# Performance work log

Measured on AMD Instinct MI355X. Metric: run time of the kernel, lower is better.

## Reference

```python
import jax, jax.numpy as jnp
import numpy as np

D = 1024
HEADS = 16
HEAD_DIM = D // HEADS
B = 4
L = 1024


def setup_inputs() -> dict:
    key = jax.random.key(0)
    kq, kk, kv, kw, kb = jax.random.split(key, 5)
    Q = jax.random.normal(kq, (B, L, D), dtype=jnp.float32)
    K = jax.random.normal(kk, (B, L, D), dtype=jnp.float32)
    V = jax.random.normal(kv, (B, L, D), dtype=jnp.float32)
    # Output projection H: torch nn.Linear(D, D) -> weight (D, D), bias (D,)
    lim = 1.0 / np.sqrt(D)
    W_H = jax.random.uniform(kw, (D, D), minval=-lim, maxval=lim, dtype=jnp.float32)
    b_H = jax.random.uniform(kb, (D,), minval=-lim, maxval=lim, dtype=jnp.float32)
    mask = 0  # falsy -> no masking branch, matching `if mask` in the source
    return {"Q": Q, "K": K, "V": V, "W_H": W_H, "b_H": b_H, "mask": mask}


def reference(Q, K, V, W_H, b_H, mask):
    batch, q_len, _ = Q.shape
    k_len = K.shape[1]
    Qh = Q.reshape(batch, q_len, HEADS, HEAD_DIM)
    Kh = K.reshape(batch, k_len, HEADS, HEAD_DIM)
    Vh = V.reshape(batch, k_len, HEADS, HEAD_DIM)
    scores = jnp.einsum('bqhd,bkhd->bhqk', Qh, Kh)  # [B,H,Lq,Lk]
    if mask:  # mask is a Python scalar (0 -> skip), as in source
        scores = jnp.where(mask == 0, -jnp.inf, scores)
    # NOTE: source scales by sqrt(D), not sqrt(head_dim)
    attn = jax.nn.softmax(scores / np.sqrt(D).astype(np.float32), axis=3)
    out = jnp.einsum('bhql,blhd->bqhd', attn, Vh).reshape(batch, q_len, D)
    return out @ W_H.T + b_H
```

## Files before the change

### kernel.cpp

```cpp
#include <hip/hip_runtime.h>
#include <hip/hip_bf16.h>

typedef __attribute__((ext_vector_type(4))) float f32x4;
typedef __attribute__((ext_vector_type(8))) short bf16x8;

constexpr int Bn  = 4;
constexpr int Ln  = 1024;
constexpr int Dn  = 1024;
constexpr int Hn  = 16;
constexpr int HDn = 64;

static __device__ __forceinline__ unsigned short bf16r(float f) {
    union { float f; unsigned int u; } x;
    x.f = f;
    unsigned int r = x.u + 0x7fffu + ((x.u >> 16) & 1u);
    return (unsigned short)(r >> 16);
}

static __device__ __forceinline__ unsigned int pk2(float a, float b) {
    return (unsigned int)bf16r(a) | ((unsigned int)bf16r(b) << 16);
}

__global__ __launch_bounds__(256) void prep_kernel(
    const float* __restrict__ Kg, const float* __restrict__ Vg,
    const float* __restrict__ Wg, unsigned short* __restrict__ Kbf,
    unsigned short* __restrict__ Vtg, unsigned short* __restrict__ Wbf)
{
    const int tid = threadIdx.x;
    if (blockIdx.z == 4) {
        const int r0 = blockIdx.x * 64, c0 = blockIdx.y * 64;
#pragma unroll 4
        for (int i = 0; i < 4; ++i) {
            int e4 = i * 256 + tid;
            int r = e4 >> 4, c4 = e4 & 15;
            const float* p = Wg + (size_t)(r0 + r) * Dn + c0 + c4 * 4;
            float4 v = *(const float4*)p;
            ushort4 o;
            o.x = bf16r(v.x); o.y = bf16r(v.y); o.z = bf16r(v.z); o.w = bf16r(v.w);
            *(ushort4*)(Wbf + (size_t)(r0 + r) * Dn + c0 + c4 * 4) = o;
        }
        return;
    }

    __shared__ unsigned short T[64][72];
    const int k0 = blockIdx.x * 64;
    const int h  = blockIdx.y;
    const int b  = blockIdx.z;
    const float* Kb = Kg + (size_t)b * Ln * Dn + h * HDn;
    const float* Vb = Vg + (size_t)b * Ln * Dn + h * HDn;
    unsigned short* Ko = Kbf + (size_t)b * Ln * Dn + h * HDn;

#pragma unroll 4
    for (int i = 0; i < 4; ++i) {
        int e4 = i * 256 + tid;
        int r = e4 >> 4, c4 = e4 & 15;
        float4 kv = *(const float4*)(Kb + (size_t)(k0 + r) * Dn + c4 * 4);
        ushort4 o;
        o.x = bf16r(kv.x); o.y = bf16r(kv.y); o.z = bf16r(kv.z); o.w = bf16r(kv.w);
        *(ushort4*)(Ko + (size_t)(k0 + r) * Dn + c4 * 4) = o;
        float4 vv = *(const float4*)(Vb + (size_t)(k0 + r) * Dn + c4 * 4);
        T[c4 * 4 + 0][r] = bf16r(vv.x);
        T[c4 * 4 + 1][r] = bf16r(vv.y);
        T[c4 * 4 + 2][r] = bf16r(vv.z);
        T[c4 * 4 + 3][r] = bf16r(vv.w);
    }
    __syncthreads();
    unsigned short* out = Vtg + ((size_t)(b * Hn + h) * HDn) * Ln + k0;
#pragma unroll 2
    for (int i = 0; i < 2; ++i) {
        int e8 = i * 256 + tid;
        int r = e8 >> 3, c8 = e8 & 7;
        *(uint4*)(out + (size_t)r * Ln + c8 * 8) = *(const uint4*)&T[r][c8 * 8];
    }
}

__global__ __launch_bounds__(512) void attn_kernel(
    const float* __restrict__ Qg, const unsigned short* __restrict__ Kbf,
    const unsigned short* __restrict__ Vtg, unsigned short* __restrict__ Xg)
{
    __shared__ uint4 Ks4[64][9];
    __shared__ uint4 Vts4[64][9];
    __shared__ uint2 Ps2[256][18];

    const int tid  = threadIdx.x;
    const int wave = tid >> 6;
    const int lane = tid & 63;
    const int l16  = lane & 15;
    const int quad = lane >> 4;
    const int wb   = wave * 32;

    const int flat = blockIdx.x;
    const int xcd  = flat & 7;
    const int j    = flat >> 3;
    const int qt   = j & 3;
    const int gg   = j >> 2;
    const int g    = xcd + 8 * gg;
    const int h    = g & 15;
    const int b    = g >> 4;
    const int q0   = qt * 256;

    const uint4* Kb4  = (const uint4*)(Kbf + (size_t)b * Ln * Dn + h * HDn);
    const uint4* Vtb4 = (const uint4*)(Vtg + ((size_t)(b * Hn + h) * HDn) * Ln);

    bf16x8 bq[2][2];
#pragma unroll 2
    for (int hf = 0; hf < 2; ++hf) {
        const float* qp = Qg + ((size_t)b * Ln + q0 + wb + hf * 16 + l16) * Dn
                             + h * HDn + quad * 8;
        float4 a0 = *(const float4*)qp;
        float4 a1 = *(const float4*)(qp + 4);
        float4 a2 = *(const float4*)(qp + 32);
        float4 a3 = *(const float4*)(qp + 36);
        bq[hf][0][0] = (short)bf16r(a0.x); bq[hf][0][1] = (short)bf16r(a0.y);
        bq[hf][0][2] = (short)bf16r(a0.z); bq[hf][0][3] = (short)bf16r(a0.w);
        bq[hf][0][4] = (short)bf16r(a1.x); bq[hf][0][5] = (short)bf16r(a1.y);
        bq[hf][0][6] = (short)bf16r(a1.z); bq[hf][0][7] = (short)bf16r(a1.w);
        bq[hf][1][0] = (short)bf16r(a2.x); bq[hf][1][1] = (short)bf16r(a2.y);
        bq[hf][1][2] = (short)bf16r(a2.z); bq[hf][1][3] = (short)bf16r(a2.w);
        bq[hf][1][4] = (short)bf16r(a3.x); bq[hf][1][5] = (short)bf16r(a3.y);
        bq[hf][1][6] = (short)bf16r(a3.z); bq[hf][1][7] = (short)bf16r(a3.w);
    }

    const float SC = 1.4426950408889634f / 32.0f;

    float lsum[2] = {0.f, 0.f};
    f32x4 Oacc[2][4];
#pragma unroll 2
    for (int hf = 0; hf < 2; ++hf)
#pragma unroll 4
        for (int d = 0; d < 4; ++d) Oacc[hf][d] = (f32x4){0.f, 0.f, 0.f, 0.f};

    const int sr = tid >> 3, sc = tid & 7;
    uint4 kreg, vreg;
    {
        kreg = Kb4[(size_t)sr * 128 + sc];
        vreg = Vtb4[(size_t)sr * 128 + sc];
    }

    for (int it = 0; it < Ln / 64; ++it) {
        __syncthreads();
        Ks4[sr][sc]  = kreg;
        Vts4[sr][sc] = vreg;
        if (it + 1 < Ln / 64) {
            kreg = Kb4[(size_t)(((it + 1) * 64) + sr) * 128 + sc];
            vreg = Vtb4[(size_t)sr * 128 + (it + 1) * 8 + sc];
        }
        __syncthreads();

        f32x4 st[2][4];
        __builtin_amdgcn_s_setprio(1);
#pragma unroll 4
        for (int n = 0; n < 4; ++n) {
            bf16x8 a0 = *(const bf16x8*)&Ks4[n * 16 + l16][quad];
            bf16x8 a1 = *(const bf16x8*)&Ks4[n * 16 + l16][4 + quad];
#pragma unroll 2
            for (int hf = 0; hf < 2; ++hf) {
                f32x4 acc = (f32x4){0.f, 0.f, 0.f, 0.f};
                acc = __builtin_amdgcn_mfma_f32_16x16x32_bf16(a0, bq[hf][0], acc, 0, 0, 0);
                acc = __builtin_amdgcn_mfma_f32_16x16x32_bf16(a1, bq[hf][1], acc, 0, 0, 0);
                st[hf][n] = acc;
            }
        }
        __builtin_amdgcn_s_setprio(0);

#pragma unroll 2
        for (int hf = 0; hf < 2; ++hf) {
            float ls = 0.f;
#pragma unroll 4
            for (int n = 0; n < 4; ++n) {
                float p0 = __builtin_amdgcn_exp2f(st[hf][n][0] * SC);
                float p1 = __builtin_amdgcn_exp2f(st[hf][n][1] * SC);
                float p2 = __builtin_amdgcn_exp2f(st[hf][n][2] * SC);
                float p3 = __builtin_amdgcn_exp2f(st[hf][n][3] * SC);
                ls += (p0 + p1) + (p2 + p3);
                uint2 w;
                w.x = pk2(p0, p1);
                w.y = pk2(p2, p3);
                Ps2[wb + hf * 16 + l16][n * 4 + quad] = w;
            }
            lsum[hf] += ls;
        }

        __builtin_amdgcn_s_setprio(1);
#pragma unroll 2
        for (int kk = 0; kk < 2; ++kk) {
            bf16x8 bv[4];
#pragma unroll 4
            for (int dt = 0; dt < 4; ++dt)
                bv[dt] = *(const bf16x8*)&Vts4[dt * 16 + l16][kk * 4 + quad];
#pragma unroll 2
            for (int hf = 0; hf < 2; ++hf) {
                bf16x8 ap = *(const bf16x8*)&Ps2[wb + hf * 16 + l16][kk * 8 + quad * 2];
#pragma unroll 4
                for (int dt = 0; dt < 4; ++dt)
                    Oacc[hf][dt] = __builtin_amdgcn_mfma_f32_16x16x32_bf16(
                        ap, bv[dt], Oacc[hf][dt], 0, 0, 0);
            }
        }
        __builtin_amdgcn_s_setprio(0);
    }

    float inv[2];
#pragma unroll 2
    for (int hf = 0; hf < 2; ++hf) {
        float rs = lsum[hf];
        rs += __shfl_xor(rs, 16, 64);
        rs += __shfl_xor(rs, 32, 64);
        inv[hf] = __builtin_amdgcn_rcpf(rs);
    }

    unsigned short* Xb = Xg + ((size_t)b * Ln + q0 + wb) * Dn + h * HDn;
#pragma unroll 2
    for (int hf = 0; hf < 2; ++hf)
#pragma unroll 4
        for (int r = 0; r < 4; ++r) {
            float iv = __shfl(inv[hf], quad * 4 + r, 64);
            int row = hf * 16 + quad * 4 + r;
#pragma unroll 4
            for (int dt = 0; dt < 4; ++dt)
                Xb[(size_t)row * Dn + dt * 16 + l16] = bf16r(Oacc[hf][dt][r] * iv);
        }
}

__global__ __launch_bounds__(256) void proj_kernel(
    const unsigned short* __restrict__ Xg, const unsigned short* __restrict__ Wbf,
    const float* __restrict__ bg, float* __restrict__ Yg)
{
    __shared__ unsigned short Xs[64][136];
    __shared__ unsigned short Wsh[64][136];

    const int tid  = threadIdx.x;
    const int wave = tid >> 6;
    const int lane = tid & 63;
    const int l16  = lane & 15;
    const int quad = lane >> 4;
    const int mw   = (wave & 1) * 32;
    const int nw   = (wave >> 1) * 32;

    const int m0 = blockIdx.x * 64;
    const int n0 = blockIdx.y * 64;

    f32x4 acc[2][2];
#pragma unroll 2
    for (int mt = 0; mt < 2; ++mt)
#pragma unroll 2
        for (int nt = 0; nt < 2; ++nt)
            acc[mt][nt] = (f32x4){0.f, 0.f, 0.f, 0.f};

    for (int it = 0; it < Dn / 128; ++it) {
        const int kk0 = it * 128;
        __syncthreads();
#pragma unroll 4
        for (int i = 0; i < 4; ++i) {
            int idx = i * 256 + tid;
            int r = idx >> 4, c8 = idx & 15;
            *(uint4*)&Xs[r][c8 * 8] =
                *(const uint4*)(Xg + (size_t)(m0 + r) * Dn + kk0 + c8 * 8);
            *(uint4*)&Wsh[r][c8 * 8] =
                *(const uint4*)(Wbf + (size_t)(n0 + r) * Dn + kk0 + c8 * 8);
        }
        __syncthreads();

#pragma unroll 4
        for (int kk = 0; kk < 4; ++kk) {
            bf16x8 af[2], bfr[2];
#pragma unroll 2
            for (int mt = 0; mt < 2; ++mt)
                af[mt] = *(const bf16x8*)&Xs[mw + mt * 16 + l16][kk * 32 + quad * 8];
#pragma unroll 2
            for (int nt = 0; nt < 2; ++nt)
                bfr[nt] = *(const bf16x8*)&Wsh[nw + nt * 16 + l16][kk * 32 + quad * 8];
#pragma unroll 2
            for (int mt = 0; mt < 2; ++mt)
#pragma unroll 2
                for (int nt = 0; nt < 2; ++nt)
                    acc[mt][nt] = __builtin_amdgcn_mfma_f32_16x16x32_bf16(
                        af[mt], bfr[nt], acc[mt][nt], 0, 0, 0);
        }
    }

#pragma unroll 2
    for (int nt = 0; nt < 2; ++nt) {
        int col = n0 + nw + nt * 16 + l16;
        float bb = bg[col];
#pragma unroll 2
        for (int mt = 0; mt < 2; ++mt)
#pragma unroll 4
            for (int r = 0; r < 4; ++r) {
                int row = m0 + mw + mt * 16 + quad * 4 + r;
                Yg[(size_t)row * Dn + col] = acc[mt][nt][r] + bb;
            }
    }
}

extern "C" void kernel_launch(void* const* d_in, const int* in_sizes, int n_in,
                              void* d_out, int out_size, void* d_ws, size_t ws_size,
                              hipStream_t stream) {
    const float* Q    = (const float*)d_in[0];
    const float* K    = (const float*)d_in[1];
    const float* V    = (const float*)d_in[2];
    const float* W    = (const float*)d_in[3];
    const float* bias = (const float*)d_in[4];

    unsigned short* Kbf = (unsigned short*)d_ws;
    unsigned short* Vt  = Kbf + (size_t)Bn * Ln * Dn;
    unsigned short* Wbf = Vt  + (size_t)Bn * Ln * Dn;
    unsigned short* X   = Wbf + (size_t)Dn * Dn;
    float* Y = (float*)d_out;

    dim3 gp(Ln / 64, Hn, Bn + 1);
    prep_kernel<<<gp, 256, 0, stream>>>(K, V, W, Kbf, Vt, Wbf);

    attn_kernel<<<dim3(256, 1, 1), 512, 0, stream>>>(Q, Kbf, Vt, X);

    dim3 g2((Bn * Ln) / 64, Dn / 64);
    proj_kernel<<<g2, 256, 0, stream>>>(X, Wbf, bias, Y);
}
```

Baseline: 148.9 us.

## Enlarge projection GEMM tile and load tiles via direct global-to-LDS

The output projection kernel now uses a 128x64 output tile per block with each wave computing 64x32, and a K-step of 64 instead of 128. Global tiles are loaded with global_load_lds straight into unpadded LDS, skipping the register round trip, and MFMA sections run at raised wave priority. The aim is more reuse per loaded byte and less load overhead. The cost is twice as many sync iterations, possible LDS bank conflicts from the unpadded layout, and fewer blocks in the grid.

After: 151.2 us. About the same (+1.6%).

```diff
diff --git a/kernel.cpp b/kernel.cpp
--- a/kernel.cpp
+++ b/kernel.cpp
@@ -226,65 +226,78 @@
     const unsigned short* __restrict__ Xg, const unsigned short* __restrict__ Wbf,
     const float* __restrict__ bg, float* __restrict__ Yg)
 {
-    __shared__ unsigned short Xs[64][136];
-    __shared__ unsigned short Wsh[64][136];
+    __shared__ unsigned short XsL[128 * 64];
+    __shared__ unsigned short WsL[64 * 64];
 
     const int tid  = threadIdx.x;
     const int wave = tid >> 6;
     const int lane = tid & 63;
     const int l16  = lane & 15;
     const int quad = lane >> 4;
-    const int mw   = (wave & 1) * 32;
+    const int mw   = (wave & 1) * 64;
     const int nw   = (wave >> 1) * 32;
 
-    const int m0 = blockIdx.x * 64;
+    const int m0 = blockIdx.x * 128;
     const int n0 = blockIdx.y * 64;
 
-    f32x4 acc[2][2];
-#pragma unroll 2
-    for (int mt = 0; mt < 2; ++mt)
+    f32x4 acc[4][2];
+#pragma unroll 4
+    for (int mt = 0; mt < 4; ++mt)
 #pragma unroll 2
         for (int nt = 0; nt < 2; ++nt)
             acc[mt][nt] = (f32x4){0.f, 0.f, 0.f, 0.f};
 
-    for (int it = 0; it < Dn / 128; ++it) {
-        const int kk0 = it * 128;
+    for (int it = 0; it < Dn / 64; ++it) {
+        const int kk0 = it * 64;
         __syncthreads();
 #pragma unroll 4
         for (int i = 0; i < 4; ++i) {
-            int idx = i * 256 + tid;
-            int r = idx >> 4, c8 = idx & 15;
-            *(uint4*)&Xs[r][c8 * 8] =
-                *(const uint4*)(Xg + (size_t)(m0 + r) * Dn + kk0 + c8 * 8);
-            *(uint4*)&Wsh[r][c8 * 8] =
-                *(const uint4*)(Wbf + (size_t)(n0 + r) * Dn + kk0 + c8 * 8);
+            int fl = i * 256 + tid;
+            int r = fl >> 3, c8 = fl & 7;
+            __builtin_amdgcn_global_load_lds(
+                (const __attribute__((address_space(1))) void*)
+                    (Xg + (size_t)(m0 + r) * Dn + kk0 + c8 * 8),
+                (__attribute__((address_space(3))) void*)&XsL[fl * 8],
+                16, 0, 0);
+        }
+#pragma unroll 2
+        for (int i = 0; i < 2; ++i) {
+            int fl = i * 256 + tid;
+            int r = fl >> 3, c8 = fl & 7;
+            __builtin_amdgcn_global_load_lds(
+                (const __attribute__((address_space(1))) void*)
+                    (Wbf + (size_t)(n0 + r) * Dn + kk0 + c8 * 8),
+                (__attribute__((address_space(3))) void*)&WsL[fl * 8],
+                16, 0, 0);
         }
         __syncthreads();
 
-#pragma unroll 4
-        for (int kk = 0; kk < 4; ++kk) {
-            bf16x8 af[2], bfr[2];
-#pragma unroll 2
-            for (int mt = 0; mt < 2; ++mt)
-                af[mt] = *(const bf16x8*)&Xs[mw + mt * 16 + l16][kk * 32 + quad * 8];
+        __builtin_amdgcn_s_setprio(1);
+#pragma unroll 2
+        for (int ks = 0; ks < 2; ++ks) {
+            bf16x8 af[4], bfr[2];
+#pragma unroll 4
+            for (int mt = 0; mt < 4; ++mt)
+                af[mt] = *(const bf16x8*)&XsL[(mw + mt * 16 + l16) * 64 + ks * 32 + quad * 8];
 #pragma unroll 2
             for (int nt = 0; nt < 2; ++nt)
-                bfr[nt] = *(const bf16x8*)&Wsh[nw + nt * 16 + l16][kk * 32 + quad * 8];
-#pragma unroll 2
-            for (int mt = 0; mt < 2; ++mt)
+                bfr[nt] = *(const bf16x8*)&WsL[(nw + nt * 16 + l16) * 64 + ks * 32 + quad * 8];
+#pragma unroll 4
+            for (int mt = 0; mt < 4; ++mt)
 #pragma unroll 2
                 for (int nt = 0; nt < 2; ++nt)
                     acc[mt][nt] = __builtin_amdgcn_mfma_f32_16x16x32_bf16(
                         af[mt], bfr[nt], acc[mt][nt], 0, 0, 0);
         }
+        __builtin_amdgcn_s_setprio(0);
     }
 
 #pragma unroll 2
     for (int nt = 0; nt < 2; ++nt) {
         int col = n0 + nw + nt * 16 + l16;
         float bb = bg[col];
-#pragma unroll 2
-        for (int mt = 0; mt < 2; ++mt)
+#pragma unroll 4
+        for (int mt = 0; mt < 4; ++mt)
 #pragma unroll 4
             for (int r = 0; r < 4; ++r) {
                 int row = m0 + mw + mt * 16 + quad * 4 + r;
@@ -313,6 +326,6 @@
 
     attn_kernel<<<dim3(256, 1, 1), 512, 0, stream>>>(Q, Kbf, Vt, X);
 
-    dim3 g2((Bn * Ln) / 64, Dn / 64);
+    dim3 g2(Bn * Ln / 128, Dn / 64);
     proj_kernel<<<g2, 256, 0, stream>>>(X, Wbf, bias, Y);
 }
```
